# Kernel tuning notes

Hardware: AMD Instinct MI355X
Metric: run time of the kernel (lower is better)

## Reference

```python
import jax, jax.numpy as jnp
import numpy as np

NEG_SLOPE = 0.01  # torch F.leaky_relu default


def _safediv(a, b):
    b = jnp.where(b == 0, jnp.ones_like(b), b)
    return a / b


def setup_inputs() -> dict:
    key = jax.random.key(0)
    ks = jax.random.split(key, 5)
    N, K, IN, HID, OUT = 50000, 32, 128, 128, 128
    h_node = jax.random.normal(ks[0], (N, IN), dtype=jnp.float32)
    h_ngbrs = jax.random.normal(ks[1], (N, K, IN), dtype=jnp.float32)
    alpha = jax.random.uniform(ks[2], (N, K, 1), dtype=jnp.float32)
    # xavier_uniform with relu gain, biases zero (as in the torch init)
    gain = float(np.sqrt(2.0))
    lim_q = gain * np.sqrt(6.0 / (IN + HID))
    lim_w = gain * np.sqrt(6.0 / (IN + HID + OUT))
    Wq = jax.random.uniform(ks[3], (HID, IN), dtype=jnp.float32, minval=-lim_q, maxval=lim_q)
    Ww = jax.random.uniform(ks[4], (OUT, IN + HID), dtype=jnp.float32, minval=-lim_w, maxval=lim_w)
    bq = jnp.zeros((HID,), dtype=jnp.float32)
    bw = jnp.zeros((OUT,), dtype=jnp.float32)
    return {"h_node": h_node, "h_ngbrs": h_ngbrs, "alpha": alpha,
            "Wq": Wq, "bq": bq, "Ww": Ww, "bw": bw}


def reference(h_node, h_ngbrs, alpha, Wq, bq, Ww, bw):
    # h_ngbrs: [N, K, IN] -> LeakyReLU(Q(h_ngbrs)): [N, K, HID]
    h1 = jax.nn.leaky_relu(jnp.einsum('nki,hi->nkh', h_ngbrs, Wq) + bq, NEG_SLOPE)
    # weighted mean over neighbors: alpha [N, K, 1]
    h_agg = _safediv((alpha * h1).sum(axis=1), alpha.sum(axis=1))  # [N, HID]
    h_concat = jnp.concatenate([h_node, h_agg], axis=-1)           # [N, IN+HID]
    h2 = jax.nn.leaky_relu(h_concat @ Ww.T + bw, NEG_SLOPE)        # [N, OUT]
    nrm = jnp.linalg.norm(h2, axis=-1, keepdims=True)              # per-node L2 norm
    return _safediv(h2, nrm)
```

## Files before the change

kernel.cpp:

```cpp
#include <hip/hip_runtime.h>

#define NNODES 50000
#define DIN 128
#define DHID 128
#define DOUT 128
#define NEG_SLOPE 0.01f
#define NT 12500
#define GG 256

typedef _Float16 f16x8 __attribute__((ext_vector_type(8)));
typedef _Float16 f16x4 __attribute__((ext_vector_type(4)));
typedef _Float16 f16x2 __attribute__((ext_vector_type(2)));
typedef float f32x4 __attribute__((ext_vector_type(4)));

__device__ __forceinline__ f16x2 pkrtz(float a, float b) {
    return __builtin_bit_cast(f16x2, __builtin_amdgcn_cvt_pkrtz(a, b));
}

#define WS_WQ_HI 0
#define WS_WQ_LO 16384
#define WS_WW_HI 32768
#define WS_WW_LO 65536

__device__ __forceinline__ void gload_lds16(const float* g, float* lds) {
    __builtin_amdgcn_global_load_lds(
        (const __attribute__((address_space(1))) void*)g,
        (__attribute__((address_space(3))) void*)lds, 16, 0, 0);
}

__global__ void convert_weights(const float* __restrict__ Wq,
                                const float* __restrict__ Ww,
                                _Float16* __restrict__ ws) {
    int id = blockIdx.x * 256 + threadIdx.x;
    if (id < 2048) {
        int s  = id;
        int l  = s & 63;
        int g  = (s >> 6) & 3;
        int ct = s >> 8;
        int col = ct * 16 + (l & 15);
        int k0  = g * 32 + (l >> 4) * 8;
        const float* src = Wq + col * DIN + k0;
        f16x8 vh, vl;
#pragma unroll
        for (int j = 0; j < 8; ++j) {
            float v = src[j];
            _Float16 h = (_Float16)v;
            vh[j] = h;
            vl[j] = (_Float16)(v - (float)h);
        }
        *(f16x8*)(ws + WS_WQ_HI + s * 8) = vh;
        *(f16x8*)(ws + WS_WQ_LO + s * 8) = vl;
    } else if (id < 2048 + 4096) {
        int s  = id - 2048;
        int l  = s & 63;
        int g  = (s >> 6) & 7;
        int ct = s >> 9;
        int col = ct * 16 + (l & 15);
        int k0  = g * 32 + (l >> 4) * 8;
        const float* src = Ww + col * (DIN + DHID) + k0;
        f16x8 vh, vl;
#pragma unroll
        for (int j = 0; j < 8; ++j) {
            float v = src[j];
            _Float16 h = (_Float16)v;
            vh[j] = h;
            vl[j] = (_Float16)(v - (float)h);
        }
        *(f16x8*)(ws + WS_WW_HI + s * 8) = vh;
        *(f16x8*)(ws + WS_WW_LO + s * 8) = vl;
    }
}

__global__ __launch_bounds__(512, 2) void gemm1_agg(
    const float* __restrict__ hng,
    const float* __restrict__ alpha,
    const float* __restrict__ bq,
    const _Float16* __restrict__ ws,
    float* __restrict__ hagg)
{
    __shared__ float As[4][4096];

    const int tid = threadIdx.x;
    const int l   = tid & 63;
    const int wid = tid >> 6;
    const int wr  = wid >> 2;
    const int wc  = wid & 3;
    const int r16 = l & 15;
    const int kg  = l >> 4;
    const int srow = l >> 3;
    const int scol = ((l & 7) ^ srow) * 4;

    const _Float16* wqh = ws + WS_WQ_HI;
    const _Float16* wql = ws + WS_WQ_LO;

    f16x8 bh[4][2], bl[4][2];
#pragma unroll
    for (int c = 0; c < 4; ++c)
#pragma unroll
        for (int ct = 0; ct < 2; ++ct) {
            int off = (((wc * 2 + ct) * 4 + c) * 64 + l) * 8;
            bh[c][ct] = *(const f16x8*)(wqh + off);
            bl[c][ct] = *(const f16x8*)(wql + off);
        }

    const float* hb = hng + (wid * 8 + srow) * DIN + scol;

#define STAGE(Rb, c)                                                          \
    do {                                                                      \
        gload_lds16(hb + (Rb)*DIN + (c) * 32, &As[c][(wid * 8) * 32]);        \
        gload_lds16(hb + ((Rb) + 64) * DIN + (c) * 32,                        \
                    &As[c][(64 + wid * 8) * 32]);                             \
    } while (0)

#define COMPUTE(c)                                                            \
    do {                                                                      \
        _Pragma("unroll")                                                     \
        for (int rt_ = 0; rt_ < 4; ++rt_) {                                   \
            int row_ = wr * 64 + rt_ * 16 + r16;                              \
            int sw_  = (r16 & 7) << 4;                                        \
            const char* rb_ = (const char*)&As[c][row_ * 32];                 \
            f32x4 v0_ = *(const f32x4*)(rb_ + ((kg * 32 + 0) ^ sw_));         \
            f32x4 v1_ = *(const f32x4*)(rb_ + ((kg * 32 + 16) ^ sw_));        \
            f16x2 p0_ = pkrtz(v0_[0], v0_[1]);                                \
            f16x2 p1_ = pkrtz(v0_[2], v0_[3]);                                \
            f16x2 p2_ = pkrtz(v1_[0], v1_[1]);                                \
            f16x2 p3_ = pkrtz(v1_[2], v1_[3]);                                \
            f16x8 ah_;                                                        \
            ah_[0] = p0_[0]; ah_[1] = p0_[1];                                 \
            ah_[2] = p1_[0]; ah_[3] = p1_[1];                                 \
            ah_[4] = p2_[0]; ah_[5] = p2_[1];                                 \
            ah_[6] = p3_[0]; ah_[7] = p3_[1];                                 \
            _Pragma("unroll")                                                 \
            for (int ct_ = 0; ct_ < 2; ++ct_) {                               \
                acc[rt_][ct_] = __builtin_amdgcn_mfma_f32_16x16x32_f16(       \
                    ah_, bh[c][ct_], acc[rt_][ct_], 0, 0, 0);                 \
                acc[rt_][ct_] = __builtin_amdgcn_mfma_f32_16x16x32_f16(       \
                    ah_, bl[c][ct_], acc[rt_][ct_], 0, 0, 0);                 \
            }                                                                 \
        }                                                                     \
    } while (0)

    long t  = blockIdx.x;
    long R0 = t * 128;

    STAGE(R0, 0);
    STAGE(R0, 1);
    STAGE(R0, 2);
    float bqv[2];
#pragma unroll
    for (int ct = 0; ct < 2; ++ct)
        bqv[ct] = bq[wc * 32 + ct * 16 + r16];
    f32x4 av4[4];
#pragma unroll
    for (int rt = 0; rt < 4; ++rt)
        av4[rt] = *(const f32x4*)(alpha + R0 + wr * 64 + rt * 16 + kg * 4);
    asm volatile("s_waitcnt vmcnt(0)" ::: "memory");
    __builtin_amdgcn_s_barrier();
    __builtin_amdgcn_sched_barrier(0);

    for (;;) {
        const bool last = (t + GG >= NT);
        const long tn   = last ? t : t + GG;
        const long Rn   = tn * 128;

        f32x4 acc[4][2];
#pragma unroll
        for (int i = 0; i < 4; ++i)
#pragma unroll
            for (int j = 0; j < 2; ++j) acc[i][j] = (f32x4){0.f, 0.f, 0.f, 0.f};

        asm volatile("s_waitcnt vmcnt(10)" ::: "memory");
        __builtin_amdgcn_s_barrier();
        __builtin_amdgcn_sched_barrier(0);
        STAGE(R0, 3);
        __builtin_amdgcn_sched_barrier(0);
        COMPUTE(0);
        asm volatile("s_waitcnt vmcnt(10)" ::: "memory");
        __builtin_amdgcn_s_barrier();
        __builtin_amdgcn_sched_barrier(0);
        STAGE(Rn, 0);
        __builtin_amdgcn_sched_barrier(0);
        COMPUTE(1);
        asm volatile("s_waitcnt vmcnt(10)" ::: "memory");
        __builtin_amdgcn_s_barrier();
        __builtin_amdgcn_sched_barrier(0);
        STAGE(Rn, 1);
        __builtin_amdgcn_sched_barrier(0);
        COMPUTE(2);
        asm volatile("s_waitcnt vmcnt(4)" ::: "memory");
        __builtin_amdgcn_s_barrier();
        __builtin_amdgcn_sched_barrier(0);
        STAGE(Rn, 2);
        __builtin_amdgcn_sched_barrier(0);
        COMPUTE(3);
        __builtin_amdgcn_sched_barrier(0);

        {
            float part[2][2] = {{0.f, 0.f}, {0.f, 0.f}};
            float apart[2] = {0.f, 0.f};
#pragma unroll
            for (int rt = 0; rt < 4; ++rt) {
                const int nl = rt >> 1;
#pragma unroll
                for (int r = 0; r < 4; ++r) {
                    float aw = av4[rt][r];
                    apart[nl] += aw;
#pragma unroll
                    for (int ct = 0; ct < 2; ++ct) {
                        float v = acc[rt][ct][r] + bqv[ct];
                        v = (v >= 0.f) ? v : NEG_SLOPE * v;
                        part[nl][ct] += aw * v;
                    }
                }
            }
#pragma unroll
            for (int nl = 0; nl < 2; ++nl) {
                apart[nl] += __shfl_xor(apart[nl], 16);
                apart[nl] += __shfl_xor(apart[nl], 32);
#pragma unroll
                for (int ct = 0; ct < 2; ++ct) {
                    part[nl][ct] += __shfl_xor(part[nl][ct], 16);
                    part[nl][ct] += __shfl_xor(part[nl][ct], 32);
                }
            }
            if (kg < 2) {
                int nl = kg;
                long node = t * 4 + wr * 2 + nl;
                float den = apart[nl];
                if (den == 0.f) den = 1.f;
#pragma unroll
                for (int ct = 0; ct < 2; ++ct) {
                    int col = wc * 32 + ct * 16 + r16;
                    hagg[node * DHID + col] = part[nl][ct] / den;
                }
            }
        }
        __builtin_amdgcn_sched_barrier(0);
#pragma unroll
        for (int rt = 0; rt < 4; ++rt)
            av4[rt] = *(const f32x4*)(alpha + Rn + wr * 64 + rt * 16 + kg * 4);
        __builtin_amdgcn_sched_barrier(0);

        if (last) break;
        t  = tn;
        R0 = Rn;
    }

#undef STAGE
#undef COMPUTE
}

__global__ __launch_bounds__(256, 2) void gemm2_norm(
    const float* __restrict__ hnode,
    const float* __restrict__ bw,
    const _Float16* __restrict__ ws,
    float* __restrict__ out)
{
    __shared__ _Float16 Ahi[8 * 520];
    __shared__ _Float16 Bhi[8 * 512];
    __shared__ _Float16 Blo[8 * 512];
    __shared__ float bw_s[128];
    __shared__ float nbuf[2][128];

    const int tid = threadIdx.x;
    const int l   = tid & 63;
    const int wid = tid >> 6;
    const int wr  = wid >> 1, wc = wid & 1;
    const long NB = (long)blockIdx.x * 128;

    if (tid < 128) bw_s[tid] = bw[tid];

    f32x4 acc[4][4];
#pragma unroll
    for (int i = 0; i < 4; ++i)
#pragma unroll
        for (int j = 0; j < 4; ++j) acc[i][j] = (f32x4){0.f, 0.f, 0.f, 0.f};

    const _Float16* wwh = ws + WS_WW_HI;
    const _Float16* wwl = ws + WS_WW_LO;

    for (int c = 0; c < 8; ++c) {
        __syncthreads();
#pragma unroll
        for (int p = 0; p < 4; ++p) {
            int rl = p * 32 + (tid >> 3);
            long n = NB + rl;
            if (n > NNODES - 1) n = NNODES - 1;
            int kw = (tid & 7) * 4;
            int kgl = c * 32 + kw;
            const float* g = (kgl < 128) ? (hnode + n * DIN + kgl)
                                         : (out + n * DHID + (kgl - 128));
            f32x4 v = *(const f32x4*)g;
            f16x2 p0 = pkrtz(v[0], v[1]);
            f16x2 p1 = pkrtz(v[2], v[3]);
            f16x4 vh;
            vh[0] = p0[0]; vh[1] = p0[1]; vh[2] = p1[0]; vh[3] = p1[1];
            int lw  = (rl & 15) | (((kw >> 3) & 3) << 4);
            int s   = rl >> 4;
            int off = s * 520 + lw * 8 + (kw & 7);
            *(f16x4*)(Ahi + off) = vh;
        }
#pragma unroll
        for (int i = 0; i < 4; ++i) {
            int id = i * 256 + tid;
            int sb = id >> 6;
            int ls = id & 63;
            if (sb < 8) {
                *(f16x8*)(Bhi + sb * 512 + ls * 8) =
                    *(const f16x8*)(wwh + ((sb * 8 + c) * 64 + ls) * 8);
            } else {
                int ct = sb - 8;
                *(f16x8*)(Blo + ct * 512 + ls * 8) =
                    *(const f16x8*)(wwl + ((ct * 8 + c) * 64 + ls) * 8);
            }
        }
        __syncthreads();
        f16x8 ah[4], bh[4], bl[4];
#pragma unroll
        for (int rt = 0; rt < 4; ++rt) {
            int s = wr * 4 + rt;
            ah[rt] = *(const f16x8*)(Ahi + s * 520 + l * 8);
        }
#pragma unroll
        for (int ct = 0; ct < 4; ++ct) {
            int s = wc * 4 + ct;
            bh[ct] = *(const f16x8*)(Bhi + s * 512 + l * 8);
            bl[ct] = *(const f16x8*)(Blo + s * 512 + l * 8);
        }
#pragma unroll
        for (int rt = 0; rt < 4; ++rt)
#pragma unroll
            for (int ct = 0; ct < 4; ++ct) {
                acc[rt][ct] = __builtin_amdgcn_mfma_f32_16x16x32_f16(ah[rt], bh[ct], acc[rt][ct], 0, 0, 0);
                acc[rt][ct] = __builtin_amdgcn_mfma_f32_16x16x32_f16(ah[rt], bl[ct], acc[rt][ct], 0, 0, 0);
            }
    }

    const int grp = l >> 4;
#pragma unroll
    for (int rt = 0; rt < 4; ++rt)
#pragma unroll
        for (int ct = 0; ct < 4; ++ct)
#pragma unroll
            for (int r = 0; r < 4; ++r) {
                int col = wc * 64 + ct * 16 + (l & 15);
                float v = acc[rt][ct][r] + bw_s[col];
                acc[rt][ct][r] = (v >= 0.f) ? v : NEG_SLOPE * v;
            }
    float ssq[4][4];
#pragma unroll
    for (int rt = 0; rt < 4; ++rt)
#pragma unroll
        for (int r = 0; r < 4; ++r) {
            float s = 0.f;
#pragma unroll
            for (int ct = 0; ct < 4; ++ct) s += acc[rt][ct][r] * acc[rt][ct][r];
            s += __shfl_xor(s, 1);
            s += __shfl_xor(s, 2);
            s += __shfl_xor(s, 4);
            s += __shfl_xor(s, 8);
            ssq[rt][r] = s;
        }
    if ((l & 15) == 0) {
#pragma unroll
        for (int rt = 0; rt < 4; ++rt)
#pragma unroll
            for (int r = 0; r < 4; ++r)
                nbuf[wc][wr * 64 + rt * 16 + grp * 4 + r] = ssq[rt][r];
    }
    __syncthreads();
#pragma unroll
    for (int rt = 0; rt < 4; ++rt)
#pragma unroll
        for (int r = 0; r < 4; ++r) {
            int rowl = wr * 64 + rt * 16 + grp * 4 + r;
            long n = NB + rowl;
            if (n < NNODES) {
                float nrm = sqrtf(nbuf[0][rowl] + nbuf[1][rowl]);
                if (nrm == 0.f) nrm = 1.f;
#pragma unroll
                for (int ct = 0; ct < 4; ++ct) {
                    int col = wc * 64 + ct * 16 + (l & 15);
                    out[n * DOUT + col] = acc[rt][ct][r] / nrm;
                }
            }
        }
}

extern "C" void kernel_launch(void* const* d_in, const int* in_sizes, int n_in,
                              void* d_out, int out_size, void* d_ws, size_t ws_size,
                              hipStream_t stream) {
    const float* h_node  = (const float*)d_in[0];
    const float* h_ngbrs = (const float*)d_in[1];
    const float* alpha   = (const float*)d_in[2];
    const float* Wq      = (const float*)d_in[3];
    const float* bq      = (const float*)d_in[4];
    const float* Ww      = (const float*)d_in[5];
    const float* bw      = (const float*)d_in[6];
    float* out   = (float*)d_out;
    _Float16* ws = (_Float16*)d_ws;

    convert_weights<<<24, 256, 0, stream>>>(Wq, Ww, ws);
    gemm1_agg<<<GG, 512, 0, stream>>>(h_ngbrs, alpha, bq, ws, out);
    gemm2_norm<<<391, 256, 0, stream>>>(h_node, bw, ws, out);
}
```

Measured before the change: 228.6 us.

## Restructure gemm1 pipeline to stage one node per chunk with triple buffering

The aggregation GEMM now stages a full node (32 neighbours × 128 features) per LDS buffer instead of splitting 128 rows by K-chunks, using a 3-slot ring of buffers rather than 4. Each wave computes 16 rows across all K, and per-node partial sums are combined across the two row groups through a small LDS exchange with an extra barrier. The aim is to cut LDS footprint (allowing more occupancy) and shorten accumulator register pressure, at the cost of an added barrier and LDS round trip per node.

Result: slower. 335.0 us (+46.5%).

```diff
diff --git a/kernel.cpp b/kernel.cpp
--- a/kernel.cpp
+++ b/kernel.cpp
@@ -78,49 +78,63 @@
     const _Float16* __restrict__ ws,
     float* __restrict__ hagg)
 {
-    __shared__ float As[4][4096];
-
-    const int tid = threadIdx.x;
-    const int l   = tid & 63;
-    const int wid = tid >> 6;
-    const int wr  = wid >> 2;
-    const int wc  = wid & 3;
-    const int r16 = l & 15;
-    const int kg  = l >> 4;
-    const int srow = l >> 3;
-    const int scol = ((l & 7) ^ srow) * 4;
+    __shared__ float As[3][4096];
+    __shared__ float px[2][4][2][16];
+    __shared__ float pxa[2];
+
+    const int tid  = threadIdx.x;
+    const int l    = tid & 63;
+    const int wid  = tid >> 6;
+    const int rgrp = wid >> 2;
+    const int cgrp = wid & 3;
+    const int r16  = l & 15;
+    const int kg   = l >> 4;
 
     const _Float16* wqh = ws + WS_WQ_HI;
     const _Float16* wql = ws + WS_WQ_LO;
 
     f16x8 bh[4][2], bl[4][2];
 #pragma unroll
-    for (int c = 0; c < 4; ++c)
+    for (int kf = 0; kf < 4; ++kf)
 #pragma unroll
         for (int ct = 0; ct < 2; ++ct) {
-            int off = (((wc * 2 + ct) * 4 + c) * 64 + l) * 8;
-            bh[c][ct] = *(const f16x8*)(wqh + off);
-            bl[c][ct] = *(const f16x8*)(wql + off);
-        }
-
-    const float* hb = hng + (wid * 8 + srow) * DIN + scol;
-
-#define STAGE(Rb, c)                                                          \
+            int off = (((cgrp * 2 + ct) * 4 + kf) * 64 + l) * 8;
+            bh[kf][ct] = *(const f16x8*)(wqh + off);
+            bl[kf][ct] = *(const f16x8*)(wql + off);
+        }
+
+    int so[2];
+#pragma unroll
+    for (int i = 0; i < 2; ++i) {
+        int rr = wid * 4 + i * 2 + (l >> 5);
+        int o  = (l & 31) * 16;
+        so[i]  = rr * 128 + (((o ^ ((rr & 7) << 4))) >> 2);
+    }
+
+    const int arow = rgrp * 16 + r16;
+    const int asw  = (arow & 7) << 4;
+
+    float bqv[2];
+#pragma unroll
+    for (int ct = 0; ct < 2; ++ct)
+        bqv[ct] = bq[cgrp * 32 + ct * 16 + r16];
+
+#define STAGE(node, s)                                                        \
     do {                                                                      \
-        gload_lds16(hb + (Rb)*DIN + (c) * 32, &As[c][(wid * 8) * 32]);        \
-        gload_lds16(hb + ((Rb) + 64) * DIN + (c) * 32,                        \
-                    &As[c][(64 + wid * 8) * 32]);                             \
+        const float* gb_ = hng + (long)(node) * 4096;                         \
+        char* lb_ = (char*)&As[s][0];                                         \
+        gload_lds16(gb_ + so[0], (float*)(lb_ + (wid * 2 + 0) * 1024));       \
+        gload_lds16(gb_ + so[1], (float*)(lb_ + (wid * 2 + 1) * 1024));       \
     } while (0)
 
-#define COMPUTE(c)                                                            \
+#define COMPUTE(s)                                                            \
     do {                                                                      \
+        const char* sb_ = (const char*)&As[s][0] + arow * 512;                \
         _Pragma("unroll")                                                     \
-        for (int rt_ = 0; rt_ < 4; ++rt_) {                                   \
-            int row_ = wr * 64 + rt_ * 16 + r16;                              \
-            int sw_  = (r16 & 7) << 4;                                        \
-            const char* rb_ = (const char*)&As[c][row_ * 32];                 \
-            f32x4 v0_ = *(const f32x4*)(rb_ + ((kg * 32 + 0) ^ sw_));         \
-            f32x4 v1_ = *(const f32x4*)(rb_ + ((kg * 32 + 16) ^ sw_));        \
+        for (int kf_ = 0; kf_ < 4; ++kf_) {                                   \
+            int kb_ = kf_ * 128 + kg * 32;                                    \
+            f32x4 v0_ = *(const f32x4*)(sb_ + ((kb_ + 0) ^ asw));             \
+            f32x4 v1_ = *(const f32x4*)(sb_ + ((kb_ + 16) ^ asw));            \
             f16x2 p0_ = pkrtz(v0_[0], v0_[1]);                                \
             f16x2 p1_ = pkrtz(v0_[2], v0_[3]);                                \
             f16x2 p2_ = pkrtz(v1_[0], v1_[1]);                                \
@@ -132,122 +146,96 @@
             ah_[6] = p3_[0]; ah_[7] = p3_[1];                                 \
             _Pragma("unroll")                                                 \
             for (int ct_ = 0; ct_ < 2; ++ct_) {                               \
-                acc[rt_][ct_] = __builtin_amdgcn_mfma_f32_16x16x32_f16(       \
-                    ah_, bh[c][ct_], acc[rt_][ct_], 0, 0, 0);                 \
-                acc[rt_][ct_] = __builtin_amdgcn_mfma_f32_16x16x32_f16(       \
-                    ah_, bl[c][ct_], acc[rt_][ct_], 0, 0, 0);                 \
+                acc[ct_] = __builtin_amdgcn_mfma_f32_16x16x32_f16(            \
+                    ah_, bh[kf_][ct_], acc[ct_], 0, 0, 0);                    \
+                acc[ct_] = __builtin_amdgcn_mfma_f32_16x16x32_f16(            \
+                    ah_, bl[kf_][ct_], acc[ct_], 0, 0, 0);                    \
             }                                                                 \
         }                                                                     \
     } while (0)
 
-    long t  = blockIdx.x;
-    long R0 = t * 128;
-
-    STAGE(R0, 0);
-    STAGE(R0, 1);
-    STAGE(R0, 2);
-    float bqv[2];
-#pragma unroll
-    for (int ct = 0; ct < 2; ++ct)
-        bqv[ct] = bq[wc * 32 + ct * 16 + r16];
-    f32x4 av4[4];
-#pragma unroll
-    for (int rt = 0; rt < 4; ++rt)
-        av4[rt] = *(const f32x4*)(alpha + R0 + wr * 64 + rt * 16 + kg * 4);
+#define CHUNK(n, nstage, nnext, scmp, sstg)                                   \
+    do {                                                                      \
+        f32x4 acc[2];                                                         \
+        acc[0] = (f32x4){0.f, 0.f, 0.f, 0.f};                                 \
+        acc[1] = (f32x4){0.f, 0.f, 0.f, 0.f};                                 \
+        asm volatile("s_waitcnt vmcnt(6)" ::: "memory");                      \
+        __builtin_amdgcn_s_barrier();                                         \
+        __builtin_amdgcn_sched_barrier(0);                                    \
+        STAGE(nstage, sstg);                                                  \
+        __builtin_amdgcn_sched_barrier(0);                                    \
+        COMPUTE(scmp);                                                        \
+          \
+        {                                                                     \
+            float p0_ = 0.f, p1_ = 0.f, ap_ = 0.f;                            \
+            _Pragma("unroll")                                                 \
+            for (int r_ = 0; r_ < 4; ++r_) {                                  \
+                float aw_ = av4[r_];                                          \
+                ap_ += aw_;                                                   \
+                float v_ = acc[0][r_] + bqv[0];                               \
+                v_ = (v_ >= 0.f) ? v_ : NEG_SLOPE * v_;                       \
+                p0_ += aw_ * v_;                                              \
+                v_ = acc[1][r_] + bqv[1];                                     \
+                v_ = (v_ >= 0.f) ? v_ : NEG_SLOPE * v_;                       \
+                p1_ += aw_ * v_;                                              \
+            }                                                                 \
+            p0_ += __shfl_xor(p0_, 16); p0_ += __shfl_xor(p0_, 32);           \
+            p1_ += __shfl_xor(p1_, 16); p1_ += __shfl_xor(p1_, 32);           \
+            ap_ += __shfl_xor(ap_, 16); ap_ += __shfl_xor(ap_, 32);           \
+            if (l < 16) {                                                     \
+                px[rgrp][cgrp][0][l] = p0_;                                   \
+                px[rgrp][cgrp][1][l] = p1_;                                   \
+            }                                                                 \
+            if (l == 0 && cgrp == 0) pxa[rgrp] = ap_;                         \
+            asm volatile("s_waitcnt lgkmcnt(0)" ::: "memory");                \
+            __builtin_amdgcn_s_barrier();                                     \
+            __builtin_amdgcn_sched_barrier(0);                                \
+            if (l < 16) {                                                     \
+                float tot_ = px[0][cgrp][rgrp][l] + px[1][cgrp][rgrp][l];     \
+                float den_ = pxa[0] + pxa[1];                                 \
+                if (den_ == 0.f) den_ = 1.f;                                  \
+                hagg[(long)(n) * DHID + cgrp * 32 + rgrp * 16 + l] =          \
+                    tot_ / den_;                                              \
+            }                                                                 \
+            av4 = *(const f32x4*)(alpha + (long)(nnext) * 32 + rgrp * 16 +    \
+                                  kg * 4);                                    \
+            __builtin_amdgcn_sched_barrier(0);                                \
+        }                                                                     \
+    } while (0)
+
+    long t = blockIdx.x;
+
+    STAGE(t * 4 + 0, 0);
+    STAGE(t * 4 + 1, 1);
+    f32x4 av4 = *(const f32x4*)(alpha + (long)(t * 4) * 32 + rgrp * 16 + kg * 4);
     asm volatile("s_waitcnt vmcnt(0)" ::: "memory");
     __builtin_amdgcn_s_barrier();
     __builtin_amdgcn_sched_barrier(0);
 
+    int sl = 0;
     for (;;) {
         const bool last = (t + GG >= NT);
         const long tn   = last ? t : t + GG;
-        const long Rn   = tn * 128;
-
-        f32x4 acc[4][2];
-#pragma unroll
-        for (int i = 0; i < 4; ++i)
-#pragma unroll
-            for (int j = 0; j < 2; ++j) acc[i][j] = (f32x4){0.f, 0.f, 0.f, 0.f};
-
-        asm volatile("s_waitcnt vmcnt(10)" ::: "memory");
-        __builtin_amdgcn_s_barrier();
-        __builtin_amdgcn_sched_barrier(0);
-        STAGE(R0, 3);
-        __builtin_amdgcn_sched_barrier(0);
-        COMPUTE(0);
-        asm volatile("s_waitcnt vmcnt(10)" ::: "memory");
-        __builtin_amdgcn_s_barrier();
-        __builtin_amdgcn_sched_barrier(0);
-        STAGE(Rn, 0);
-        __builtin_amdgcn_sched_barrier(0);
-        COMPUTE(1);
-        asm volatile("s_waitcnt vmcnt(10)" ::: "memory");
-        __builtin_amdgcn_s_barrier();
-        __builtin_amdgcn_sched_barrier(0);
-        STAGE(Rn, 1);
-        __builtin_amdgcn_sched_barrier(0);
-        COMPUTE(2);
-        asm volatile("s_waitcnt vmcnt(4)" ::: "memory");
-        __builtin_amdgcn_s_barrier();
-        __builtin_amdgcn_sched_barrier(0);
-        STAGE(Rn, 2);
-        __builtin_amdgcn_sched_barrier(0);
-        COMPUTE(3);
-        __builtin_amdgcn_sched_barrier(0);
-
-        {
-            float part[2][2] = {{0.f, 0.f}, {0.f, 0.f}};
-            float apart[2] = {0.f, 0.f};
-#pragma unroll
-            for (int rt = 0; rt < 4; ++rt) {
-                const int nl = rt >> 1;
-#pragma unroll
-                for (int r = 0; r < 4; ++r) {
-                    float aw = av4[rt][r];
-                    apart[nl] += aw;
-#pragma unroll
-                    for (int ct = 0; ct < 2; ++ct) {
-                        float v = acc[rt][ct][r] + bqv[ct];
-                        v = (v >= 0.f) ? v : NEG_SLOPE * v;
-                        part[nl][ct] += aw * v;
-                    }
-                }
-            }
-#pragma unroll
-            for (int nl = 0; nl < 2; ++nl) {
-                apart[nl] += __shfl_xor(apart[nl], 16);
-                apart[nl] += __shfl_xor(apart[nl], 32);
-#pragma unroll
-                for (int ct = 0; ct < 2; ++ct) {
-                    part[nl][ct] += __shfl_xor(part[nl][ct], 16);
-                    part[nl][ct] += __shfl_xor(part[nl][ct], 32);
-                }
-            }
-            if (kg < 2) {
-                int nl = kg;
-                long node = t * 4 + wr * 2 + nl;
-                float den = apart[nl];
-                if (den == 0.f) den = 1.f;
-#pragma unroll
-                for (int ct = 0; ct < 2; ++ct) {
-                    int col = wc * 32 + ct * 16 + r16;
-                    hagg[node * DHID + col] = part[nl][ct] / den;
-                }
-            }
-        }
-        __builtin_amdgcn_sched_barrier(0);
-#pragma unroll
-        for (int rt = 0; rt < 4; ++rt)
-            av4[rt] = *(const f32x4*)(alpha + Rn + wr * 64 + rt * 16 + kg * 4);
-        __builtin_amdgcn_sched_barrier(0);
+        const long n0   = t * 4;
+        const long m0   = tn * 4;
+        const int s0 = sl;
+        const int s1 = (sl + 1 > 2) ? sl - 2 : sl + 1;
+        const int s2 = (sl + 2 > 2) ? sl - 1 : sl + 2;
+
+        CHUNK(n0 + 0, n0 + 2, n0 + 1, s0, s2);
+        CHUNK(n0 + 1, n0 + 3, n0 + 2, s1, s0);
+        CHUNK(n0 + 2, m0 + 0, n0 + 3, s2, s1);
+        CHUNK(n0 + 3, m0 + 1, m0 + 0, s0, s2);
 
         if (last) break;
         t  = tn;
-        R0 = Rn;
-    }
+        sl = s1;
+    }
+    asm volatile("s_waitcnt vmcnt(0)" ::: "memory");
 
 #undef STAGE
 #undef COMPUTE
+#undef CHUNK
 }
 
 __global__ __launch_bounds__(256, 2) void gemm2_norm(
```

## Double-buffer full 128-row tiles instead of a four-chunk K ring

Applied to the files above, without the earlier changes.

The first kernel now stages a whole 128x128 fp32 tile of neighbour features per iteration into one of two LDS buffers, using swizzled per-thread offsets. The previous scheme staged four K-chunks with a barrier between each. Each iteration now issues the next tile's loads once, then runs all four K-steps of MFMA on the current buffer. The goal is fewer barriers and waitcnt stalls and deeper prefetch per block. The cost is doubling LDS to 128KB per block, which leaves room for only one resident block per CU.

New measurement: 232.8 us. Within noise of the previous version (+1.8%).

```diff
diff --git a/kernel.cpp b/kernel.cpp
--- a/kernel.cpp
+++ b/kernel.cpp
@@ -78,7 +78,7 @@
     const _Float16* __restrict__ ws,
     float* __restrict__ hagg)
 {
-    __shared__ float As[4][4096];
+    __shared__ float As[2][16384];
 
     const int tid = threadIdx.x;
     const int l   = tid & 63;
@@ -87,55 +87,70 @@
     const int wc  = wid & 3;
     const int r16 = l & 15;
     const int kg  = l >> 4;
-    const int srow = l >> 3;
-    const int scol = ((l & 7) ^ srow) * 4;
 
     const _Float16* wqh = ws + WS_WQ_HI;
     const _Float16* wql = ws + WS_WQ_LO;
 
     f16x8 bh[4][2], bl[4][2];
 #pragma unroll
-    for (int c = 0; c < 4; ++c)
+    for (int kf = 0; kf < 4; ++kf)
 #pragma unroll
         for (int ct = 0; ct < 2; ++ct) {
-            int off = (((wc * 2 + ct) * 4 + c) * 64 + l) * 8;
-            bh[c][ct] = *(const f16x8*)(wqh + off);
-            bl[c][ct] = *(const f16x8*)(wql + off);
-        }
-
-    const float* hb = hng + (wid * 8 + srow) * DIN + scol;
-
-#define STAGE(Rb, c)                                                          \
+            int off = (((wc * 2 + ct) * 4 + kf) * 64 + l) * 8;
+            bh[kf][ct] = *(const f16x8*)(wqh + off);
+            bl[kf][ct] = *(const f16x8*)(wql + off);
+        }
+
+    int so[8];
+#pragma unroll
+    for (int i = 0; i < 8; ++i) {
+        int row = (wid * 8 + i) * 2 + (l >> 5);
+        int o   = (l & 31) * 16;
+        so[i]   = row * 128 + ((o ^ ((row & 7) << 4)) >> 2);
+    }
+
+    float bqv[2];
+#pragma unroll
+    for (int ct = 0; ct < 2; ++ct)
+        bqv[ct] = bq[wc * 32 + ct * 16 + r16];
+
+#define STAGE(Rb, s)                                                          \
     do {                                                                      \
-        gload_lds16(hb + (Rb)*DIN + (c) * 32, &As[c][(wid * 8) * 32]);        \
-        gload_lds16(hb + ((Rb) + 64) * DIN + (c) * 32,                        \
-                    &As[c][(64 + wid * 8) * 32]);                             \
+        _Pragma("unroll")                                                     \
+        for (int i_ = 0; i_ < 8; ++i_) {                                      \
+            gload_lds16(hng + (long)(Rb)*DIN + so[i_],                        \
+                        &As[s][(wid * 8 + i_) * 256]);                        \
+        }                                                                     \
     } while (0)
 
-#define COMPUTE(c)                                                            \
+#define COMPUTE(s)                                                            \
     do {                                                                      \
         _Pragma("unroll")                                                     \
         for (int rt_ = 0; rt_ < 4; ++rt_) {                                   \
             int row_ = wr * 64 + rt_ * 16 + r16;                              \
-            int sw_  = (r16 & 7) << 4;                                        \
-            const char* rb_ = (const char*)&As[c][row_ * 32];                 \
-            f32x4 v0_ = *(const f32x4*)(rb_ + ((kg * 32 + 0) ^ sw_));         \
-            f32x4 v1_ = *(const f32x4*)(rb_ + ((kg * 32 + 16) ^ sw_));        \
-            f16x2 p0_ = pkrtz(v0_[0], v0_[1]);                                \
-            f16x2 p1_ = pkrtz(v0_[2], v0_[3]);                                \
-            f16x2 p2_ = pkrtz(v1_[0], v1_[1]);                                \
-            f16x2 p3_ = pkrtz(v1_[2], v1_[3]);                                \
-            f16x8 ah_;                                                        \
-            ah_[0] = p0_[0]; ah_[1] = p0_[1];                                 \
-            ah_[2] = p1_[0]; ah_[3] = p1_[1];                                 \
-            ah_[4] = p2_[0]; ah_[5] = p2_[1];                                 \
-            ah_[6] = p3_[0]; ah_[7] = p3_[1];                                 \
+            int asw_ = (row_ & 7) << 4;                                       \
+            const char* sb_ = (const char*)&As[s][0] + row_ * 512;            \
             _Pragma("unroll")                                                 \
-            for (int ct_ = 0; ct_ < 2; ++ct_) {                               \
-                acc[rt_][ct_] = __builtin_amdgcn_mfma_f32_16x16x32_f16(       \
-                    ah_, bh[c][ct_], acc[rt_][ct_], 0, 0, 0);                 \
-                acc[rt_][ct_] = __builtin_amdgcn_mfma_f32_16x16x32_f16(       \
-                    ah_, bl[c][ct_], acc[rt_][ct_], 0, 0, 0);                 \
+            for (int kf_ = 0; kf_ < 4; ++kf_) {                               \
+                int kb_ = kf_ * 128 + kg * 32;                                \
+                f32x4 v0_ = *(const f32x4*)(sb_ + ((kb_ + 0) ^ asw_));        \
+                f32x4 v1_ = *(const f32x4*)(sb_ + ((kb_ + 16) ^ asw_));       \
+                f16x2 p0_ = pkrtz(v0_[0], v0_[1]);                            \
+                f16x2 p1_ = pkrtz(v0_[2], v0_[3]);                            \
+                f16x2 p2_ = pkrtz(v1_[0], v1_[1]);                            \
+                f16x2 p3_ = pkrtz(v1_[2], v1_[3]);                            \
+                f16x8 ah_;                                                    \
+                ah_[0] = p0_[0]; ah_[1] = p0_[1];                             \
+                ah_[2] = p1_[0]; ah_[3] = p1_[1];                             \
+                ah_[4] = p2_[0]; ah_[5] = p2_[1];                             \
+                ah_[6] = p3_[0]; ah_[7] = p3_[1];                             \
+                _Pragma("unroll")                                             \
+                for (int ct_ = 0; ct_ < 2; ++ct_) {                           \
+                    acc[rt_][ct_] = __builtin_amdgcn_mfma_f32_16x16x32_f16(   \
+                        ah_, bh[kf_][ct_], acc[rt_][ct_], 0, 0, 0);           \
+                    acc[rt_][ct_] = __builtin_amdgcn_mfma_f32_16x16x32_f16(   \
+                        ah_, bl[kf_][ct_], acc[rt_][ct_], 0, 0, 0);           \
+                }                                                             \
             }                                                                 \
         }                                                                     \
     } while (0)
@@ -144,12 +159,6 @@
     long R0 = t * 128;
 
     STAGE(R0, 0);
-    STAGE(R0, 1);
-    STAGE(R0, 2);
-    float bqv[2];
-#pragma unroll
-    for (int ct = 0; ct < 2; ++ct)
-        bqv[ct] = bq[wc * 32 + ct * 16 + r16];
     f32x4 av4[4];
 #pragma unroll
     for (int rt = 0; rt < 4; ++rt)
@@ -158,6 +167,7 @@
     __builtin_amdgcn_s_barrier();
     __builtin_amdgcn_sched_barrier(0);
 
+    int cur = 0;
     for (;;) {
         const bool last = (t + GG >= NT);
         const long tn   = last ? t : t + GG;
@@ -169,30 +179,12 @@
 #pragma unroll
             for (int j = 0; j < 2; ++j) acc[i][j] = (f32x4){0.f, 0.f, 0.f, 0.f};
 
-        asm volatile("s_waitcnt vmcnt(10)" ::: "memory");
+        asm volatile("s_waitcnt vmcnt(6)" ::: "memory");
         __builtin_amdgcn_s_barrier();
         __builtin_amdgcn_sched_barrier(0);
-        STAGE(R0, 3);
+        STAGE(Rn, cur ^ 1);
         __builtin_amdgcn_sched_barrier(0);
-        COMPUTE(0);
-        asm volatile("s_waitcnt vmcnt(10)" ::: "memory");
-        __builtin_amdgcn_s_barrier();
-        __builtin_amdgcn_sched_barrier(0);
-        STAGE(Rn, 0);
-        __builtin_amdgcn_sched_barrier(0);
-        COMPUTE(1);
-        asm volatile("s_waitcnt vmcnt(10)" ::: "memory");
-        __builtin_amdgcn_s_barrier();
-        __builtin_amdgcn_sched_barrier(0);
-        STAGE(Rn, 1);
-        __builtin_amdgcn_sched_barrier(0);
-        COMPUTE(2);
-        asm volatile("s_waitcnt vmcnt(4)" ::: "memory");
-        __builtin_amdgcn_s_barrier();
-        __builtin_amdgcn_sched_barrier(0);
-        STAGE(Rn, 2);
-        __builtin_amdgcn_sched_barrier(0);
-        COMPUTE(3);
+        COMPUTE(cur);
         __builtin_amdgcn_sched_barrier(0);
 
         {
@@ -242,9 +234,11 @@
         __builtin_amdgcn_sched_barrier(0);
 
         if (last) break;
-        t  = tn;
-        R0 = Rn;
+        t   = tn;
+        R0  = Rn;
+        cur ^= 1;
     }
+    asm volatile("s_waitcnt vmcnt(0)" ::: "memory");
 
 #undef STAGE
 #undef COMPUTE
```
